# Performance work log

Hardware: AMD Instinct MI355X
Metric: run time of the kernel (lower is better)

Reference implementation:

```python
import jax, jax.numpy as jnp
import numpy as np

NUM_HEADS = 8
DIM_HEAD = 64
EMBED = NUM_HEADS * DIM_HEAD  # 512
B, S, L = 2, 128, 128


def setup_inputs() -> dict:
    key = jax.random.key(0)
    k1, k2 = jax.random.split(key)
    x = jax.random.normal(k1, (B, EMBED, S, L), dtype=jnp.float32)
    # 1x1 Conv2d == pointwise linear over channels: weight [3E, E], bias [3E]
    W = jax.random.normal(k2, (3 * EMBED, EMBED), dtype=jnp.float32) * (EMBED ** -0.5)
    b = jnp.zeros((3 * EMBED,), dtype=jnp.float32)
    return {"x": x, "W": W, "b": b}


def reference(x, W, b):
    Bsz, D, S_, L_ = x.shape
    H, Dh = NUM_HEADS, DIM_HEAD
    scale = Dh ** -0.5
    # QKV projection (1x1 conv)
    qkv = jnp.einsum('oi,bisl->bosl', W, x) + b[None, :, None, None]
    q, k, v = jnp.split(qkv, 3, axis=1)
    q = q.reshape(Bsz, H, Dh, S_, L_) * scale
    k = k.reshape(Bsz, H, Dh, S_, L_)
    v = v.reshape(Bsz, H, Dh, S_, L_)
    # Column attention: attend along S axis, independently per column l
    col_scores = jnp.einsum('bhdsl,bhdtl->bhlst', q, k)      # [B,H,L,S,S]
    col_attn = jax.nn.softmax(col_scores, axis=-1)
    out_col = jnp.einsum('bhlst,bhdtl->bhdsl', col_attn, v)  # [B,H,Dh,S,L]
    # Row attention: attend along L axis, independently per row s
    row_scores = jnp.einsum('bhdsl,bhdsm->bhslm', q, k)      # [B,H,S,L,L]
    row_attn = jax.nn.softmax(row_scores, axis=-1)
    out_row = jnp.einsum('bhslm,bhdsm->bhdsl', row_attn, v)  # [B,H,Dh,S,L]
    out = (out_col + out_row).reshape(Bsz, H * Dh, S_, L_)
    return out
```

## Files before the change

### kernel.cpp

```cpp
#include <hip/hip_runtime.h>
#include <stdint.h>

#define EMB 512
#define THREE_E 1536
#define SL 16384
#define K_DIM 512

typedef unsigned short ushort;
typedef short bf16x8 __attribute__((ext_vector_type(8)));
typedef float f32x4 __attribute__((ext_vector_type(4)));

__device__ __forceinline__ ushort f2bf(float f) {
  unsigned u = __float_as_uint(f);
  u += 0x7fffu + ((u >> 16) & 1u);
  return (ushort)(u >> 16);
}
__device__ __forceinline__ float bf2f(ushort s) {
  return __uint_as_float((unsigned)s << 16);
}

__device__ __forceinline__ void async16(const ushort* g, ushort* l) {
  __builtin_amdgcn_global_load_lds(
      (const __attribute__((address_space(1))) unsigned int*)g,
      (__attribute__((address_space(3))) unsigned int*)l, 16, 0, 0);
}

__global__ __launch_bounds__(256) void wconv(const float* __restrict__ W,
                                             ushort* __restrict__ Wb) {
  int i = blockIdx.x * 256 + threadIdx.x;
  float4 f = ((const float4*)W)[i];
  uint2 o;
  o.x = (unsigned)f2bf(f.x) | ((unsigned)f2bf(f.y) << 16);
  o.y = (unsigned)f2bf(f.z) | ((unsigned)f2bf(f.w) << 16);
  ((uint2*)Wb)[i] = o;
}

__global__ __launch_bounds__(256) void xpose(const float* __restrict__ x,
                                             ushort* __restrict__ xT) {
  __shared__ ushort t[64][65];
  int b = blockIdx.z;
  int i0 = blockIdx.y * 64;
  int n0 = blockIdx.x * 64;
  int c = threadIdx.x & 63;
  int r0 = threadIdx.x >> 6;
  const float* xp = x + ((size_t)(b * EMB + i0)) * SL + n0;
  #pragma unroll
  for (int rr = 0; rr < 16; rr++) {
    int r = r0 * 16 + rr;
    t[r][c] = f2bf(xp[(size_t)r * SL + c]);
  }
  __syncthreads();
  ushort* op = xT + ((size_t)(b * SL + n0)) * EMB + i0;
  #pragma unroll
  for (int rr = 0; rr < 16; rr++) {
    int rn = r0 * 16 + rr;
    op[(size_t)rn * EMB + c] = t[c][rn];
  }
}

__global__ __launch_bounds__(256) void qkv_gemm(const ushort* __restrict__ Wb,
                                                const ushort* __restrict__ xT,
                                                const float* __restrict__ bias,
                                                ushort* __restrict__ rowQ) {
  __shared__ __align__(16) char sm[34816];
  ushort* As = (ushort*)sm;
  ushort* Bs = (ushort*)(sm + 16384);
  const int tid = threadIdx.x;
  const int b = blockIdx.z;
  const int m0 = blockIdx.y * 128;
  const int n0 = blockIdx.x * 128;
  const int lane = tid & 63;
  const int w = tid >> 6;
  const int wr = (w >> 1) * 64;
  const int wc = (w & 1) * 64;
  const int l15 = lane & 15;
  const int quad = lane >> 4;
  const ushort* xb = xT + (size_t)b * SL * EMB;
  f32x4 acc[4][4] = {};
  const int r8 = lane >> 3;
  const int cg = (lane & 7) ^ r8;
  for (int k0 = 0; k0 < K_DIM; k0 += 64) {
    __syncthreads();
    #pragma unroll
    for (int t = 0; t < 4; t++) {
      int seg = 4 * w + t;
      int row = seg * 8 + r8;
      async16(&Wb[(size_t)(m0 + row) * K_DIM + k0 + cg * 8], &As[seg * 512]);
      async16(&xb[(size_t)(n0 + row) * K_DIM + k0 + cg * 8], &Bs[seg * 512]);
    }
    __syncthreads();
    #pragma unroll
    for (int ks = 0; ks < 2; ks++) {
      bf16x8 av[4], bv[4];
      #pragma unroll
      for (int mt = 0; mt < 4; mt++) {
        int row = wr + mt * 16 + l15;
        av[mt] = *(const bf16x8*)&As[row * 64 + (((ks * 4 + quad) ^ (row & 7)) * 8)];
      }
      #pragma unroll
      for (int nt = 0; nt < 4; nt++) {
        int row = wc + nt * 16 + l15;
        bv[nt] = *(const bf16x8*)&Bs[row * 64 + (((ks * 4 + quad) ^ (row & 7)) * 8)];
      }
      #pragma unroll
      for (int mt = 0; mt < 4; mt++)
        #pragma unroll
        for (int nt = 0; nt < 4; nt++)
          acc[mt][nt] = __builtin_amdgcn_mfma_f32_16x16x32_bf16(av[mt], bv[nt], acc[mt][nt], 0, 0, 0);
    }
  }
  __syncthreads();
  {
    ushort* epi = (ushort*)sm;
    const float sc = (m0 < EMB) ? 0.125f : 1.0f;
    const int q4r = quad * 4;
    #pragma unroll
    for (int mt = 0; mt < 4; mt++) {
      int mb = wr + mt * 16 + q4r;
      float b0 = bias[m0 + mb], b1 = bias[m0 + mb + 1];
      float b2 = bias[m0 + mb + 2], b3 = bias[m0 + mb + 3];
      #pragma unroll
      for (int nt = 0; nt < 4; nt++) {
        int l = wc + nt * 16 + l15;
        unsigned u0 = f2bf((acc[mt][nt][0] + b0) * sc);
        unsigned u1 = f2bf((acc[mt][nt][1] + b1) * sc);
        unsigned u2 = f2bf((acc[mt][nt][2] + b2) * sc);
        unsigned u3 = f2bf((acc[mt][nt][3] + b3) * sc);
        uint2 pk;
        pk.x = u0 | (u1 << 16);
        pk.y = u2 | (u3 << 16);
        *(uint2*)&epi[l * 136 + mb] = pk;
      }
    }
  }
  __syncthreads();
  {
    const ushort* epi = (const ushort*)sm;
    const int sel = m0 >> 9;
    const int hb = (m0 & 511) >> 6;
    const int s = blockIdx.x;
    #pragma unroll
    for (int it = 0; it < 8; it++) {
      int flat = it * 2048 + tid * 8;
      int head = flat >> 13;
      int rem = flat & 8191;
      int l = rem >> 6;
      int dd = rem & 63;
      size_t dst = ((((size_t)(b * 3 + sel) * 8 + hb + head) * 128 + s) * 128 + l) * 64 + dd;
      *(uint4*)&rowQ[dst] = *(const uint4*)&epi[l * 136 + head * 64 + dd];
    }
  }
}

__global__ __launch_bounds__(256) void attn2(const ushort* __restrict__ qkv,
                                             ushort* __restrict__ tmp,
                                             float* __restrict__ out,
                                             int colpass) {
  __shared__ ushort Qs[128 * 72];
  __shared__ ushort Ks[128 * 72];
  __shared__ ushort Vt[64 * 136];
  __shared__ ushort PsU[64 * 136];
  ushort* Ps = PsU;
  ushort* Os = PsU;
  const int tid = threadIdx.x;
  const int fixed = blockIdx.x;
  const int h = blockIdx.y, b = blockIdx.z;
  const int w = tid >> 6, lane = tid & 63, l15 = lane & 15, quad = lane >> 4;
  const size_t off = colpass ? (size_t)fixed * 64 : (size_t)fixed * 8192;
  const size_t tstr = colpass ? 8192 : 64;
  const ushort* Qg = qkv + ((size_t)(b * 3 + 0) * 8 + h) * 1048576 + off;
  const ushort* Kg = Qg + (size_t)8 * 1048576;
  const ushort* Vg = Qg + (size_t)16 * 1048576;
  ushort* tb = tmp + (size_t)(b * 8 + h) * 1048576;
  {
    int trow = tid >> 3, d0 = (tid & 7) * 8, dg = tid & 7;
    #pragma unroll
    for (int it = 0; it < 4; it++) {
      int t = trow + it * 32;
      size_t g = (size_t)t * tstr + d0;
      *(uint4*)&Qs[t * 72 + d0] = *(const uint4*)&Qg[g];
      *(uint4*)&Ks[t * 72 + d0] = *(const uint4*)&Kg[g];
      uint4 vv = *(const uint4*)&Vg[g];
      ushort* vs = (ushort*)&vv;
      #pragma unroll
      for (int k = 0; k < 8; k++) {
        int i = (k + dg) & 7;
        Vt[(d0 + i) * 136 + t] = vs[i];
      }
    }
  }
  __syncthreads();
  const int row0 = w * 16 + quad * 4;
  for (int c = 0; c < 2; c++) {
    ushort treg[16];
    if (!colpass) {
      const ushort* tp = tb + (size_t)(c * 64 + row0) * 8192 + (size_t)fixed * 64 + l15;
      #pragma unroll
      for (int r = 0; r < 4; r++)
        #pragma unroll
        for (int nt = 0; nt < 4; nt++)
          treg[r * 4 + nt] = tp[(size_t)r * 8192 + nt * 16];
    }
    const int sb = c * 64 + w * 16;
    bf16x8 aq0 = *(const bf16x8*)&Qs[(sb + l15) * 72 + quad * 8];
    bf16x8 aq1 = *(const bf16x8*)&Qs[(sb + l15) * 72 + 32 + quad * 8];
    f32x4 accS[8];
    #pragma unroll
    for (int nt = 0; nt < 8; nt++) {
      f32x4 z = {0.f, 0.f, 0.f, 0.f};
      bf16x8 bk0 = *(const bf16x8*)&Ks[(nt * 16 + l15) * 72 + quad * 8];
      bf16x8 bk1 = *(const bf16x8*)&Ks[(nt * 16 + l15) * 72 + 32 + quad * 8];
      z = __builtin_amdgcn_mfma_f32_16x16x32_bf16(aq0, bk0, z, 0, 0, 0);
      z = __builtin_amdgcn_mfma_f32_16x16x32_bf16(aq1, bk1, z, 0, 0, 0);
      accS[nt] = z;
    }
    float inv[4];
    #pragma unroll
    for (int r = 0; r < 4; r++) {
      float mx = accS[0][r];
      #pragma unroll
      for (int nt = 1; nt < 8; nt++) mx = fmaxf(mx, accS[nt][r]);
      mx = fmaxf(mx, __shfl_xor(mx, 1));
      mx = fmaxf(mx, __shfl_xor(mx, 2));
      mx = fmaxf(mx, __shfl_xor(mx, 4));
      mx = fmaxf(mx, __shfl_xor(mx, 8));
      float s = 0.f;
      #pragma unroll
      for (int nt = 0; nt < 8; nt++) {
        float p = __builtin_amdgcn_exp2f((accS[nt][r] - mx) * 1.44269504088896f);
        accS[nt][r] = p;
        s += p;
      }
      s += __shfl_xor(s, 1);
      s += __shfl_xor(s, 2);
      s += __shfl_xor(s, 4);
      s += __shfl_xor(s, 8);
      inv[r] = 1.0f / s;
    }
    #pragma unroll
    for (int nt = 0; nt < 8; nt++)
      #pragma unroll
      for (int r = 0; r < 4; r++)
        Ps[(row0 + r) * 136 + nt * 16 + l15] = f2bf(accS[nt][r]);
    __syncthreads();
    f32x4 accO[4] = {{0.f,0.f,0.f,0.f},{0.f,0.f,0.f,0.f},{0.f,0.f,0.f,0.f},{0.f,0.f,0.f,0.f}};
    #pragma unroll
    for (int kf = 0; kf < 4; kf++) {
      bf16x8 ap = *(const bf16x8*)&Ps[(w * 16 + l15) * 136 + kf * 32 + quad * 8];
      #pragma unroll
      for (int nt = 0; nt < 4; nt++) {
        bf16x8 bv = *(const bf16x8*)&Vt[(nt * 16 + l15) * 136 + kf * 32 + quad * 8];
        accO[nt] = __builtin_amdgcn_mfma_f32_16x16x32_bf16(ap, bv, accO[nt], 0, 0, 0);
      }
    }
    __syncthreads();
    #pragma unroll
    for (int nt = 0; nt < 4; nt++)
      #pragma unroll
      for (int r = 0; r < 4; r++) {
        float v = accO[nt][r] * inv[r];
        if (!colpass) v += bf2f(treg[r * 4 + nt]);
        Os[(row0 + r) * 72 + nt * 16 + l15] = f2bf(v);
      }
    __syncthreads();
    if (colpass) {
      #pragma unroll
      for (int it = 0; it < 2; it++) {
        int flat = (it * 256 + tid) * 8;
        *(uint4*)&tb[(size_t)fixed * 8192 + c * 4096 + flat] =
            *(const uint4*)&Os[(flat >> 6) * 72 + (flat & 63)];
      }
    } else {
      float* ob = out + (size_t)(b * EMB + h * 64) * SL + (size_t)fixed * 128 + c * 64;
      #pragma unroll
      for (int it = 0; it < 4; it++) {
        int f4 = it * 256 + tid;
        int d = f4 >> 4, l4 = f4 & 15;
        float4 o;
        o.x = bf2f(Os[(l4 * 4 + 0) * 72 + d]);
        o.y = bf2f(Os[(l4 * 4 + 1) * 72 + d]);
        o.z = bf2f(Os[(l4 * 4 + 2) * 72 + d]);
        o.w = bf2f(Os[(l4 * 4 + 3) * 72 + d]);
        *(float4*)&ob[(size_t)d * SL + l4 * 4] = o;
      }
    }
    __syncthreads();
  }
}

extern "C" void kernel_launch(void* const* d_in, const int* in_sizes, int n_in,
                              void* d_out, int out_size, void* d_ws, size_t ws_size,
                              hipStream_t stream) {
  const float* x = (const float*)d_in[0];
  const float* W = (const float*)d_in[1];
  const float* bias = (const float*)d_in[2];
  float* out = (float*)d_out;
  ushort* rowQ = (ushort*)d_ws;
  ushort* xT = (ushort*)((char*)d_ws + 100663296);
  ushort* tmp = (ushort*)((char*)d_ws + 100663296);
  ushort* Wb = (ushort*)((char*)d_ws + 134217728);

  hipLaunchKernelGGL(wconv, dim3(768), dim3(256), 0, stream, W, Wb);
  hipLaunchKernelGGL(xpose, dim3(256, 8, 2), dim3(256), 0, stream, x, xT);
  hipLaunchKernelGGL(qkv_gemm, dim3(128, 12, 2), dim3(256), 0, stream, Wb, xT, bias, rowQ);
  hipLaunchKernelGGL(attn2, dim3(128, 8, 2), dim3(256), 0, stream, rowQ, tmp, out, 1);
  hipLaunchKernelGGL(attn2, dim3(128, 8, 2), dim3(256), 0, stream, rowQ, tmp, out, 0);
}
```

Measured before the change: 290.3 us.

## Restructure axial attention kernel: async swizzled K load, direct Q regs, fewer barriers

Turns the attention kernel into a template over column versus row pass. K is loaded with async global-to-LDS copies into an XOR-swizzled layout, and Q fragments and the row-pass residual are read straight into registers instead of staging through shared memory. Softmax normalisation moves before the P store, and the output staging buffer and most __syncthreads barriers are dropped. Results are written directly from MFMA accumulators, with operands swapped in the row pass so the stores come out in the right orientation. This cuts LDS traffic and barrier stalls, but relies on per-wave waitcnt ordering and gives up coalesced output stores.

```diff
diff --git a/kernel.cpp b/kernel.cpp
--- a/kernel.cpp
+++ b/kernel.cpp
@@ -152,35 +152,39 @@
   }
 }
 
-__global__ __launch_bounds__(256) void attn2(const ushort* __restrict__ qkv,
+template <int COL>
+__global__ __launch_bounds__(256) void attn3(const ushort* __restrict__ qkv,
                                              ushort* __restrict__ tmp,
-                                             float* __restrict__ out,
-                                             int colpass) {
-  __shared__ ushort Qs[128 * 72];
-  __shared__ ushort Ks[128 * 72];
+                                             float* __restrict__ out) {
+  __shared__ ushort Ks[128 * 64];
   __shared__ ushort Vt[64 * 136];
-  __shared__ ushort PsU[64 * 136];
-  ushort* Ps = PsU;
-  ushort* Os = PsU;
+  __shared__ ushort Ps[64 * 136];
   const int tid = threadIdx.x;
   const int fixed = blockIdx.x;
   const int h = blockIdx.y, b = blockIdx.z;
   const int w = tid >> 6, lane = tid & 63, l15 = lane & 15, quad = lane >> 4;
-  const size_t off = colpass ? (size_t)fixed * 64 : (size_t)fixed * 8192;
-  const size_t tstr = colpass ? 8192 : 64;
+  const size_t off = COL ? (size_t)fixed * 64 : (size_t)fixed * 8192;
+  const size_t tstr = COL ? 8192 : 64;
   const ushort* Qg = qkv + ((size_t)(b * 3 + 0) * 8 + h) * 1048576 + off;
   const ushort* Kg = Qg + (size_t)8 * 1048576;
   const ushort* Vg = Qg + (size_t)16 * 1048576;
   ushort* tb = tmp + (size_t)(b * 8 + h) * 1048576;
   {
+    int r8k = lane >> 3;
+    int cgk = (lane & 7) ^ r8k;
+    #pragma unroll
+    for (int t = 0; t < 4; t++) {
+      int seg = 4 * w + t;
+      int row = seg * 8 + r8k;
+      async16(&Kg[(size_t)row * tstr + cgk * 8], &Ks[seg * 512]);
+    }
+  }
+  {
     int trow = tid >> 3, d0 = (tid & 7) * 8, dg = tid & 7;
     #pragma unroll
     for (int it = 0; it < 4; it++) {
       int t = trow + it * 32;
-      size_t g = (size_t)t * tstr + d0;
-      *(uint4*)&Qs[t * 72 + d0] = *(const uint4*)&Qg[g];
-      *(uint4*)&Ks[t * 72 + d0] = *(const uint4*)&Kg[g];
-      uint4 vv = *(const uint4*)&Vg[g];
+      uint4 vv = *(const uint4*)&Vg[(size_t)t * tstr + d0];
       ushort* vs = (ushort*)&vv;
       #pragma unroll
       for (int k = 0; k < 8; k++) {
@@ -189,29 +193,35 @@
       }
     }
   }
+  bf16x8 aq[2][2];
+  #pragma unroll
+  for (int c = 0; c < 2; c++) {
+    const ushort* qp = Qg + (size_t)(c * 64 + w * 16 + l15) * tstr + quad * 8;
+    aq[c][0] = *(const bf16x8*)qp;
+    aq[c][1] = *(const bf16x8*)(qp + 32);
+  }
+  uint2 treg[2][4];
+  if (!COL) {
+    #pragma unroll
+    for (int c = 0; c < 2; c++) {
+      const ushort* tp = tb + (size_t)(c * 64 + w * 16 + l15) * 8192 + (size_t)fixed * 64 + quad * 4;
+      #pragma unroll
+      for (int mt = 0; mt < 4; mt++) treg[c][mt] = *(const uint2*)(tp + mt * 16);
+    }
+  }
   __syncthreads();
-  const int row0 = w * 16 + quad * 4;
+  const int rx = l15 & 7;
+  #pragma unroll
   for (int c = 0; c < 2; c++) {
-    ushort treg[16];
-    if (!colpass) {
-      const ushort* tp = tb + (size_t)(c * 64 + row0) * 8192 + (size_t)fixed * 64 + l15;
-      #pragma unroll
-      for (int r = 0; r < 4; r++)
-        #pragma unroll
-        for (int nt = 0; nt < 4; nt++)
-          treg[r * 4 + nt] = tp[(size_t)r * 8192 + nt * 16];
-    }
-    const int sb = c * 64 + w * 16;
-    bf16x8 aq0 = *(const bf16x8*)&Qs[(sb + l15) * 72 + quad * 8];
-    bf16x8 aq1 = *(const bf16x8*)&Qs[(sb + l15) * 72 + 32 + quad * 8];
     f32x4 accS[8];
     #pragma unroll
     for (int nt = 0; nt < 8; nt++) {
+      int row = nt * 16 + l15;
+      bf16x8 bk0 = *(const bf16x8*)&Ks[row * 64 + ((quad ^ rx) * 8)];
+      bf16x8 bk1 = *(const bf16x8*)&Ks[row * 64 + (((quad + 4) ^ rx) * 8)];
       f32x4 z = {0.f, 0.f, 0.f, 0.f};
-      bf16x8 bk0 = *(const bf16x8*)&Ks[(nt * 16 + l15) * 72 + quad * 8];
-      bf16x8 bk1 = *(const bf16x8*)&Ks[(nt * 16 + l15) * 72 + 32 + quad * 8];
-      z = __builtin_amdgcn_mfma_f32_16x16x32_bf16(aq0, bk0, z, 0, 0, 0);
-      z = __builtin_amdgcn_mfma_f32_16x16x32_bf16(aq1, bk1, z, 0, 0, 0);
+      z = __builtin_amdgcn_mfma_f32_16x16x32_bf16(aq[c][0], bk0, z, 0, 0, 0);
+      z = __builtin_amdgcn_mfma_f32_16x16x32_bf16(aq[c][1], bk1, z, 0, 0, 0);
       accS[nt] = z;
     }
     float inv[4];
@@ -237,54 +247,41 @@
       s += __shfl_xor(s, 8);
       inv[r] = 1.0f / s;
     }
+    asm volatile("s_waitcnt lgkmcnt(0)" ::: "memory");
     #pragma unroll
     for (int nt = 0; nt < 8; nt++)
       #pragma unroll
       for (int r = 0; r < 4; r++)
-        Ps[(row0 + r) * 136 + nt * 16 + l15] = f2bf(accS[nt][r]);
-    __syncthreads();
+        Ps[(w * 16 + quad * 4 + r) * 136 + nt * 16 + l15] = f2bf(accS[nt][r] * inv[r]);
+    asm volatile("s_waitcnt lgkmcnt(0)" ::: "memory");
     f32x4 accO[4] = {{0.f,0.f,0.f,0.f},{0.f,0.f,0.f,0.f},{0.f,0.f,0.f,0.f},{0.f,0.f,0.f,0.f}};
     #pragma unroll
     for (int kf = 0; kf < 4; kf++) {
-      bf16x8 ap = *(const bf16x8*)&Ps[(w * 16 + l15) * 136 + kf * 32 + quad * 8];
-      #pragma unroll
-      for (int nt = 0; nt < 4; nt++) {
-        bf16x8 bv = *(const bf16x8*)&Vt[(nt * 16 + l15) * 136 + kf * 32 + quad * 8];
-        accO[nt] = __builtin_amdgcn_mfma_f32_16x16x32_bf16(ap, bv, accO[nt], 0, 0, 0);
-      }
-    }
-    __syncthreads();
-    #pragma unroll
-    for (int nt = 0; nt < 4; nt++)
-      #pragma unroll
-      for (int r = 0; r < 4; r++) {
-        float v = accO[nt][r] * inv[r];
-        if (!colpass) v += bf2f(treg[r * 4 + nt]);
-        Os[(row0 + r) * 72 + nt * 16 + l15] = f2bf(v);
-      }
-    __syncthreads();
-    if (colpass) {
-      #pragma unroll
-      for (int it = 0; it < 2; it++) {
-        int flat = (it * 256 + tid) * 8;
-        *(uint4*)&tb[(size_t)fixed * 8192 + c * 4096 + flat] =
-            *(const uint4*)&Os[(flat >> 6) * 72 + (flat & 63)];
-      }
+      bf16x8 p = *(const bf16x8*)&Ps[(w * 16 + l15) * 136 + kf * 32 + quad * 8];
+      #pragma unroll
+      for (int t4 = 0; t4 < 4; t4++) {
+        bf16x8 v = *(const bf16x8*)&Vt[(t4 * 16 + l15) * 136 + kf * 32 + quad * 8];
+        accO[t4] = COL ? __builtin_amdgcn_mfma_f32_16x16x32_bf16(p, v, accO[t4], 0, 0, 0)
+                       : __builtin_amdgcn_mfma_f32_16x16x32_bf16(v, p, accO[t4], 0, 0, 0);
+      }
+    }
+    if (COL) {
+      ushort* tp = tb + (size_t)fixed * 8192 + c * 4096;
+      #pragma unroll
+      for (int t4 = 0; t4 < 4; t4++)
+        #pragma unroll
+        for (int r = 0; r < 4; r++)
+          tp[(w * 16 + quad * 4 + r) * 64 + t4 * 16 + l15] = f2bf(accO[t4][r]);
     } else {
-      float* ob = out + (size_t)(b * EMB + h * 64) * SL + (size_t)fixed * 128 + c * 64;
-      #pragma unroll
-      for (int it = 0; it < 4; it++) {
-        int f4 = it * 256 + tid;
-        int d = f4 >> 4, l4 = f4 & 15;
-        float4 o;
-        o.x = bf2f(Os[(l4 * 4 + 0) * 72 + d]);
-        o.y = bf2f(Os[(l4 * 4 + 1) * 72 + d]);
-        o.z = bf2f(Os[(l4 * 4 + 2) * 72 + d]);
-        o.w = bf2f(Os[(l4 * 4 + 3) * 72 + d]);
-        *(float4*)&ob[(size_t)d * SL + l4 * 4] = o;
-      }
-    }
-    __syncthreads();
+      float* ob = out + (size_t)(b * EMB + h * 64) * SL + (size_t)fixed * 128 + c * 64 + w * 16 + l15;
+      #pragma unroll
+      for (int t4 = 0; t4 < 4; t4++) {
+        const ushort* tr = (const ushort*)&treg[c][t4];
+        #pragma unroll
+        for (int r = 0; r < 4; r++)
+          ob[(size_t)(t4 * 16 + quad * 4 + r) * SL] = accO[t4][r] + bf2f(tr[r]);
+      }
+    }
   }
 }
 
@@ -303,6 +300,6 @@
   hipLaunchKernelGGL(wconv, dim3(768), dim3(256), 0, stream, W, Wb);
   hipLaunchKernelGGL(xpose, dim3(256, 8, 2), dim3(256), 0, stream, x, xT);
   hipLaunchKernelGGL(qkv_gemm, dim3(128, 12, 2), dim3(256), 0, stream, Wb, xT, bias, rowQ);
-  hipLaunchKernelGGL(attn2, dim3(128, 8, 2), dim3(256), 0, stream, rowQ, tmp, out, 1);
-  hipLaunchKernelGGL(attn2, dim3(128, 8, 2), dim3(256), 0, stream, rowQ, tmp, out, 0);
-}
+  hipLaunchKernelGGL(attn3<1>, dim3(128, 8, 2), dim3(256), 0, stream, rowQ, tmp, out);
+  hipLaunchKernelGGL(attn3<0>, dim3(128, 8, 2), dim3(256), 0, stream, rowQ, tmp, out);
+}
```

Measured after the change: 255.4 us. -12.0%, faster.
